# Optimization experiments

Hardware: AMD Instinct MI355X
Metric: run time of the kernel (lower is better)

Reference implementation:

```python
import jax, jax.numpy as jnp
import numpy as np

K_NN = 20  # neighbors per group (k=20 in source)


def fps_one(xyz, npoint):
    # xyz: [N,3] -> indices [npoint] via iterative furthest point sampling
    N = xyz.shape[0]
    def body(carry, _):
        dist, far = carry
        d = jnp.sum((xyz - xyz[far]) ** 2, axis=-1)
        dist = jnp.minimum(dist, d)
        return (dist, jnp.argmax(dist).astype(jnp.int32)), far
    init = (jnp.full((N,), 1e10, xyz.dtype), jnp.int32(0))
    _, idx = jax.lax.scan(body, init, None, length=npoint)
    return idx


def gather(pts, idx):
    # pts: [B,M,C], idx: [B,...] -> [B,...,C]
    return jax.vmap(lambda p, i: p[i])(pts, idx)


def knn(q, ref, k):
    # q: [B,S,3], ref: [B,M,3] -> [B,S,k] indices of nearest refs
    d = (jnp.sum(q * q, -1, keepdims=True)
         - 2.0 * jnp.einsum('bsc,bmc->bsm', q, ref)
         + jnp.sum(ref * ref, -1)[:, None, :])
    _, idx = jax.lax.top_k(-d, k)
    return idx


def sa_block(xyz, feats, npoint, W, b):
    # Set abstraction: FPS sample -> kNN group -> shared MLP -> max pool
    fidx = jax.vmap(fps_one, in_axes=(0, None))(xyz, npoint)   # [B,S]
    new_xyz = gather(xyz, fidx)                                 # [B,S,3]
    nidx = knn(new_xyz, xyz, K_NN)                              # [B,S,K]
    rel = gather(xyz, nidx) - new_xyz[:, :, None, :]            # [B,S,K,3]
    grp = jnp.concatenate([rel, gather(feats, nidx)], -1)       # [B,S,K,3+C]
    h = jax.nn.relu(jnp.einsum('bskc,cd->bskd', grp, W) + b)
    return new_xyz, jnp.max(h, axis=2)                          # [B,S,Cout]


def fp_block(xq, xr, fr, skip, W, b):
    # Feature propagation: 3-NN inverse-distance interp -> concat skip -> MLP
    idx = knn(xq, xr, 3)                                        # [B,S,3]
    d = jnp.sum((gather(xr, idx) - xq[:, :, None, :]) ** 2, -1)
    w = 1.0 / (d + 1e-8)
    w = w / jnp.sum(w, -1, keepdims=True)
    interp = jnp.einsum('bsk,bskc->bsc', w, gather(fr, idx))
    cat = jnp.concatenate([interp, skip], -1)
    return jax.nn.relu(jnp.einsum('bsc,cd->bsd', cat, W) + b)


def setup_inputs() -> dict:
    key = jax.random.key(0)
    ks = jax.random.split(key, 24)
    B, N = 8, 4096
    x = jax.random.normal(ks[0], (B, 6, N), jnp.float32)
    cls_label = jax.random.uniform(ks[1], (B, 16), jnp.float32)
    def lin(k, cin, cout):
        kw, kb = jax.random.split(k)
        s = 1.0 / np.sqrt(cin)
        return (jax.random.normal(kw, (cin, cout), jnp.float32) * s,
                jax.random.normal(kb, (cout,), jnp.float32) * 0.01)
    W0, b0 = lin(ks[2], 6, 64)
    W1, b1 = lin(ks[3], 67, 128)
    W2, b2 = lin(ks[4], 131, 256)
    W3, b3 = lin(ks[5], 259, 512)
    F3, fb3 = lin(ks[6], 768, 512)
    F2, fb2 = lin(ks[7], 640, 256)
    F1, fb1 = lin(ks[8], 320, 128)
    F0, fb0 = lin(ks[9], 150, 128)
    Wseg, bseg = lin(ks[10], 128, 50)
    return {"x": x, "cls_label": cls_label,
            "W0": W0, "b0": b0, "W1": W1, "b1": b1, "W2": W2, "b2": b2,
            "W3": W3, "b3": b3, "F3": F3, "fb3": fb3, "F2": F2, "fb2": fb2,
            "F1": F1, "fb1": fb1, "F0": F0, "fb0": fb0,
            "Wseg": Wseg, "bseg": bseg}


def reference(x, cls_label, W0, b0, W1, b1, W2, b2, W3, b3,
              F3, fb3, F2, fb2, F1, fb1, F0, fb0, Wseg, bseg):
    B, _, N = x.shape
    xyz = jnp.transpose(x[:, :3, :], (0, 2, 1))   # [B,N,3]
    nrm = jnp.transpose(x[:, 3:, :], (0, 2, 1))   # [B,N,3]
    # hierarchical set abstraction (512 -> 256 -> 128 -> 64 points)
    x1, f1 = sa_block(xyz, nrm, 512, W0, b0)      # f1: [B,512,64]
    x2, f2 = sa_block(x1, f1, 256, W1, b1)        # f2: [B,256,128]
    x3, f3 = sa_block(x2, f2, 128, W2, b2)        # f3: [B,128,256]
    x4, f4 = sa_block(x3, f3, 64, W3, b3)         # f4: [B,64,512]
    # feature propagation back up
    g3 = fp_block(x3, x4, f4, f3, F3, fb3)        # [B,128,512]
    g2 = fp_block(x2, x3, g3, f2, F2, fb2)        # [B,256,256]
    g1 = fp_block(x1, x2, g2, f1, F1, fb1)        # [B,512,128]
    cls = jnp.broadcast_to(cls_label[:, None, :], (B, N, 16))
    skip0 = jnp.concatenate([cls, xyz, nrm], -1)  # [B,N,22]
    g0 = fp_block(xyz, x1, g1, skip0, F0, fb0)    # [B,N,128]
    result = jnp.einsum('bnc,cd->bnd', g0, Wseg) + bseg  # [B,N,50]
    return result, jnp.transpose(g0, (0, 2, 1))
```

## Files before the change

kernel.cpp:

```cpp
#include <hip/hip_runtime.h>
#include <float.h>

#define B8 8
#define NPTS 4096

__global__ void split_xyz_kernel(const float* __restrict__ x,
                                 float* __restrict__ xyz, float* __restrict__ nrm) {
  int g = blockIdx.x * 256 + threadIdx.x;
  if (g >= B8 * NPTS) return;
  int b = g / NPTS, n = g % NPTS;
  const float* xb = x + (size_t)b * 6 * NPTS;
  float* o1 = xyz + (size_t)g * 3;
  float* o2 = nrm + (size_t)g * 3;
  o1[0] = xb[0 * NPTS + n]; o1[1] = xb[1 * NPTS + n]; o1[2] = xb[2 * NPTS + n];
  o2[0] = xb[3 * NPTS + n]; o2[1] = xb[4 * NPTS + n]; o2[2] = xb[5 * NPTS + n];
}

template <int CTRL, int RM>
__device__ __forceinline__ unsigned dppmov(unsigned v) {
  return (unsigned)__builtin_amdgcn_update_dpp((int)v, (int)v, CTRL, RM, 0xf, false);
}

template <int CTRL, int RM>
__device__ __forceinline__ void red_key_max(unsigned& kh, unsigned& kl) {
  unsigned oh = dppmov<CTRL, RM>(kh);
  unsigned ol = dppmov<CTRL, RM>(kl);
  unsigned long long ko = ((unsigned long long)oh << 32) | ol;
  unsigned long long k  = ((unsigned long long)kh << 32) | kl;
  bool c = ko > k;
  kh = c ? oh : kh;
  kl = c ? ol : kl;
}

template <int CTRL, int RM>
__device__ __forceinline__ void red_key_min(unsigned& kh, unsigned& kl) {
  unsigned oh = dppmov<CTRL, RM>(kh);
  unsigned ol = dppmov<CTRL, RM>(kl);
  unsigned long long ko = ((unsigned long long)oh << 32) | ol;
  unsigned long long k  = ((unsigned long long)kh << 32) | kl;
  bool c = ko < k;
  kh = c ? oh : kh;
  kl = c ? ol : kl;
}

#define WAVE_RED_MAX(kh, kl)            \
  red_key_max<0x111, 0xf>(kh, kl);      \
  red_key_max<0x112, 0xf>(kh, kl);      \
  red_key_max<0x114, 0xf>(kh, kl);      \
  red_key_max<0x118, 0xf>(kh, kl);      \
  red_key_max<0x142, 0xa>(kh, kl);      \
  red_key_max<0x143, 0xc>(kh, kl);

#define WAVE_RED_MIN(kh, kl)            \
  red_key_min<0x111, 0xf>(kh, kl);      \
  red_key_min<0x112, 0xf>(kh, kl);      \
  red_key_min<0x114, 0xf>(kh, kl);      \
  red_key_min<0x118, 0xf>(kh, kl);      \
  red_key_min<0x142, 0xa>(kh, kl);      \
  red_key_min<0x143, 0xc>(kh, kl);

template <int BLOCK, int P>
__global__ __launch_bounds__(BLOCK) void fps4_kernel(const float* __restrict__ xyz,
                                                     int N, int S,
                                                     float* __restrict__ out_xyz) {
#pragma clang fp contract(off)
  constexpr int NW = BLOCK / 64;
  __shared__ float4 pts[BLOCK * P];
  __shared__ float4 sel[512];
  __shared__ alignas(16) unsigned long long wkey[2][NW];
  int b = blockIdx.x, t = threadIdx.x;
  const float* p = xyz + (size_t)b * N * 3;
  float px[P], py[P], pz[P], dist[P];
#pragma unroll
  for (int j = 0; j < P; ++j) {
    int idx = t + j * BLOCK;
    float a = p[3 * idx], bb = p[3 * idx + 1], c = p[3 * idx + 2];
    px[j] = a; py[j] = bb; pz[j] = c;
    pts[idx] = make_float4(a, bb, c, 0.f);
    dist[j] = 1e10f;
  }
  __syncthreads();
  float fx = p[0], fy = p[1], fz = p[2];
  for (int i = 0; i < S; ++i) {
    if (t == 0) sel[i] = make_float4(fx, fy, fz, 0.f);
    float bv = -1.0f;
    int bj = 0;
#pragma unroll
    for (int j = 0; j < P; ++j) {
      float dx = px[j] - fx, dy = py[j] - fy, dz = pz[j] - fz;
      float d = dx * dx + dy * dy + dz * dz;
      float nd = fminf(dist[j], d);
      dist[j] = nd;
      bool c = nd > bv;
      bv = c ? nd : bv;
      bj = c ? j : bj;
    }
    unsigned kh = __float_as_uint(bv);
    unsigned kl = (unsigned)(~(t + bj * BLOCK));
    WAVE_RED_MAX(kh, kl);
    int buf = i & 1;
    if ((t & 63) == 63)
      wkey[buf][t >> 6] = ((unsigned long long)kh << 32) | kl;
    __syncthreads();
    unsigned long long g = 0ull;
    const ulonglong2* wk2 = (const ulonglong2*)&wkey[buf][0];
#pragma unroll
    for (int w = 0; w < NW / 2; ++w) {
      ulonglong2 e = wk2[w];
      unsigned long long m = (e.x > e.y) ? e.x : e.y;
      g = (m > g) ? m : g;
    }
    int far = (int)~(unsigned)g;
    float4 f = pts[far];
    fx = f.x; fy = f.y; fz = f.z;
  }
  __syncthreads();
  for (int i = t; i < S; i += BLOCK) {
    float4 f = sel[i];
    float* o = out_xyz + ((size_t)b * S + i) * 3;
    o[0] = f.x; o[1] = f.y; o[2] = f.z;
  }
}

__global__ __launch_bounds__(64) void knn20_kernel(const float* __restrict__ q,
                                                   const float* __restrict__ ref,
                                                   int S, int M, int* __restrict__ nidx,
                                                   int LDQ, int LDR) {
#pragma clang fp contract(off)
  int bs = blockIdx.x;
  int b = bs / S, s = bs % S;
  int t = threadIdx.x;
  __shared__ float sd[4096];
  const float* qp = q + ((size_t)b * LDQ + s) * 3;
  float qx = qp[0], qy = qp[1], qz = qp[2];
  float qq = qx * qx + qy * qy + qz * qz;
  const float* rp = ref + (size_t)b * LDR * 3;
  for (int i = t; i < M; i += 64) {
    float rx = rp[3 * i], ry = rp[3 * i + 1], rz = rp[3 * i + 2];
    float rr = rx * rx + ry * ry + rz * rz;
    float dot = qx * rx + qy * ry + qz * rz;
    sd[i] = qq - 2.0f * dot + rr;
  }
  __syncthreads();
  unsigned keep = 0;
  for (int k = 0; k < 20; ++k) {
    float bv = FLT_MAX;
    int bi = 0;
    for (int i = t; i < M; i += 64) {
      float v = sd[i];
      bool c = v < bv;
      bv = c ? v : bv;
      bi = c ? i : bi;
    }
    unsigned kh = __float_as_uint(bv), kl = (unsigned)bi;
    WAVE_RED_MIN(kh, kl);
    unsigned w = (unsigned)__builtin_amdgcn_readlane((int)kl, 63);
    if (t == k) keep = w;
    if (t == 0) sd[w] = FLT_MAX;
    __syncthreads();
  }
  if (t < 20) nidx[(size_t)bs * 20 + t] = (int)keep;
}

__device__ __forceinline__ void knn3_store(int g, const float* rx3,
                                           float qx, float qy, float qz,
                                           int i0, int i1, int i2,
                                           int* __restrict__ idx3,
                                           float* __restrict__ w3) {
#pragma clang fp contract(off)
  int ii[3] = {i0, i1, i2};
  float w[3];
  float wsum = 0.0f;
#pragma unroll
  for (int k = 0; k < 3; ++k) {
    const float* r = rx3 + (size_t)ii[k] * 3;
    float dx = r[0] - qx, dy = r[1] - qy, dz = r[2] - qz;
    float d = dx * dx + dy * dy + dz * dz;
    w[k] = 1.0f / (d + 1e-8f);
    wsum += w[k];
  }
#pragma unroll
  for (int k = 0; k < 3; ++k) {
    idx3[(size_t)g * 3 + k] = ii[k];
    w3[(size_t)g * 3 + k] = w[k] / wsum;
  }
}

__global__ __launch_bounds__(256) void neighbors_kernel(
    const float* __restrict__ xyz, const float* __restrict__ x1,
    int* __restrict__ nidx2, int* __restrict__ nidx3, int* __restrict__ nidx4,
    int* __restrict__ idx3_3, float* __restrict__ w3_3,
    int* __restrict__ idx3_2, float* __restrict__ w3_2,
    int* __restrict__ idx3_1, float* __restrict__ w3_1,
    int* __restrict__ idx3_0, float* __restrict__ w3_0) {
#pragma clang fp contract(off)
  __shared__ float4 smem4[512];
  int blk = blockIdx.x, tid = threadIdx.x;

  if (blk < 896) {
    int S, M, qid;
    int* nout;
    const int wv = tid >> 6, t64 = tid & 63;
    if (blk < 512)      { S = 256; M = 512; qid = blk * 4 + wv;         nout = nidx2; }
    else if (blk < 768) { S = 128; M = 256; qid = (blk - 512) * 4 + wv; nout = nidx3; }
    else                { S = 64;  M = 128; qid = (blk - 768) * 4 + wv; nout = nidx4; }
    float* swd = (float*)smem4 + wv * M;
    int b = qid / S, s = qid % S;
    const float* qp = x1 + ((size_t)b * 512 + s) * 3;
    float qx = qp[0], qy = qp[1], qz = qp[2];
    float qq = qx * qx + qy * qy + qz * qz;
    const float* rp = x1 + (size_t)b * 512 * 3;
    for (int i = t64; i < M; i += 64) {
      float rx = rp[3 * i], ry = rp[3 * i + 1], rz = rp[3 * i + 2];
      float rr = rx * rx + ry * ry + rz * rz;
      float dot = qx * rx + qy * ry + qz * rz;
      swd[i] = qq - 2.0f * dot + rr;
    }
    __syncthreads();
    unsigned keep = 0;
    for (int k = 0; k < 20; ++k) {
      float bv = FLT_MAX;
      int bi = 0;
      for (int i = t64; i < M; i += 64) {
        float v = swd[i];
        bool c = v < bv;
        bv = c ? v : bv;
        bi = c ? i : bi;
      }
      unsigned kh = __float_as_uint(bv), kl = (unsigned)bi;
      WAVE_RED_MIN(kh, kl);
      unsigned w = (unsigned)__builtin_amdgcn_readlane((int)kl, 63);
      if (t64 == k) keep = w;
      if (t64 == 0) swd[w] = FLT_MAX;
      __syncthreads();
    }
    if (t64 < 20) nout[(size_t)qid * 20 + t64] = (int)keep;
    return;
  }

  if (blk < 900) {
    int g = (blk - 896) * 256 + tid;
    int Sq = 128, M = 64;
    int b = g / Sq, s = g % Sq;
    const float* qp = x1 + ((size_t)b * 512 + s) * 3;
    float qx = qp[0], qy = qp[1], qz = qp[2];
    float qq = qx * qx + qy * qy + qz * qz;
    const float* rp = x1 + (size_t)b * 512 * 3;
    float v0 = FLT_MAX, v1 = FLT_MAX, v2 = FLT_MAX;
    int i0 = 0, i1 = 0, i2 = 0;
    for (int i = 0; i < M; ++i) {
      float rx = rp[3 * i], ry = rp[3 * i + 1], rz = rp[3 * i + 2];
      float d = qq - 2.0f * (qx * rx + qy * ry + qz * rz) + (rx * rx + ry * ry + rz * rz);
      if (d < v2) {
        if (d < v1) {
          if (d < v0) { v2 = v1; i2 = i1; v1 = v0; i1 = i0; v0 = d; i0 = i; }
          else { v2 = v1; i2 = i1; v1 = d; i1 = i; }
        } else { v2 = d; i2 = i; }
      }
    }
    knn3_store(g, rp, qx, qy, qz, i0, i1, i2, idx3_3, w3_3);
    return;
  }

  int g, Sq, M, LDQ;
  int* oidx;
  float* ow;
  const float* q;
  if (blk < 908)      { g = (blk - 900) * 256 + tid; Sq = 256;  M = 128; oidx = idx3_2; ow = w3_2; q = x1;  LDQ = 512; }
  else if (blk < 924) { g = (blk - 908) * 256 + tid; Sq = 512;  M = 256; oidx = idx3_1; ow = w3_1; q = x1;  LDQ = 512; }
  else                { g = (blk - 924) * 256 + tid; Sq = 4096; M = 512; oidx = idx3_0; ow = w3_0; q = xyz; LDQ = 4096; }
  int b = g / Sq, s = g % Sq;
  const float* rp = x1 + (size_t)b * 512 * 3;
  for (int i = tid; i < M; i += 256) {
    float rx = rp[3 * i], ry = rp[3 * i + 1], rz = rp[3 * i + 2];
    smem4[i] = make_float4(rx, ry, rz, rx * rx + ry * ry + rz * rz);
  }
  __syncthreads();
  const float* qp = q + ((size_t)b * LDQ + s) * 3;
  float qx = qp[0], qy = qp[1], qz = qp[2];
  float qq = qx * qx + qy * qy + qz * qz;
  float v0 = FLT_MAX, v1 = FLT_MAX, v2 = FLT_MAX;
  int i0 = 0, i1 = 0, i2 = 0;
  for (int i = 0; i < M; ++i) {
    float4 r = smem4[i];
    float d = qq - 2.0f * (qx * r.x + qy * r.y + qz * r.z) + r.w;
    if (d < v2) {
      if (d < v1) {
        if (d < v0) { v2 = v1; i2 = i1; v1 = v0; i1 = i0; v0 = d; i0 = i; }
        else { v2 = v1; i2 = i1; v1 = d; i1 = i; }
      } else { v2 = d; i2 = i; }
    }
  }
  {
    int ii[3] = {i0, i1, i2};
    float w[3];
    float wsum = 0.0f;
#pragma unroll
    for (int k = 0; k < 3; ++k) {
      float4 r = smem4[ii[k]];
      float dx = r.x - qx, dy = r.y - qy, dz = r.z - qz;
      float d = dx * dx + dy * dy + dz * dz;
      w[k] = 1.0f / (d + 1e-8f);
      wsum += w[k];
    }
#pragma unroll
    for (int k = 0; k < 3; ++k) {
      oidx[(size_t)g * 3 + k] = ii[k];
      ow[(size_t)g * 3 + k] = w[k] / wsum;
    }
  }
}

#define GEMM_STAGE(k0v, ...)                                                      \
    {                                                                             \
      int r_ = (int)threadIdx.x & 63;                                             \
      int ks_ = (int)threadIdx.x >> 6;                                            \
      int rr = rowBase + r_;                                                      \
      int kq0 = (k0v) + ks_ * 4;                                                  \
      float4 va = make_float4(0.f, 0.f, 0.f, 0.f);                                \
      if (rr < Mrows) { __VA_ARGS__ }                                             \
      areg4 = va;                                                                 \
    }                                                                             \
    {                                                                             \
      int kk = (int)threadIdx.x >> 4;                                             \
      int n4 = ((int)threadIdx.x & 15) * 4;                                       \
      int kq = (k0v) + kk, cc = colBase + n4;                                     \
      if (colBase + 64 <= N) {                                                    \
        if (kq < K) breg4 = *reinterpret_cast<const float4*>(&Wm[(size_t)kq * N + cc]); \
        else breg4 = make_float4(0.f, 0.f, 0.f, 0.f);                             \
      } else {                                                                    \
        breg4.x = (kq < K && cc < N) ? Wm[(size_t)kq * N + cc] : 0.0f;            \
        breg4.y = (kq < K && cc + 1 < N) ? Wm[(size_t)kq * N + cc + 1] : 0.0f;    \
        breg4.z = (kq < K && cc + 2 < N) ? Wm[(size_t)kq * N + cc + 2] : 0.0f;    \
        breg4.w = (kq < K && cc + 3 < N) ? Wm[(size_t)kq * N + cc + 3] : 0.0f;    \
      }                                                                           \
    }

#define GEMM_WRITE_LDS(bufv)                                                      \
    {                                                                             \
      int r_ = (int)threadIdx.x & 63;                                             \
      int k4_ = ((int)threadIdx.x >> 6) * 4;                                      \
      As[bufv][k4_ + 0][r_] = areg4.x;                                            \
      As[bufv][k4_ + 1][r_] = areg4.y;                                            \
      As[bufv][k4_ + 2][r_] = areg4.z;                                            \
      As[bufv][k4_ + 3][r_] = areg4.w;                                            \
    }                                                                             \
    *reinterpret_cast<float4*>(&Bs[bufv][threadIdx.x >> 4][(threadIdx.x & 15) * 4]) = breg4;

#define GEMM_MAIN(...)                                                            \
  __shared__ alignas(16) float As[2][16][68];                                     \
  __shared__ alignas(16) float Bs[2][16][64];                                     \
  int tx = threadIdx.x & 15, ty = threadIdx.x >> 4;                               \
  int rowBase = blockIdx.y * 64;                                                  \
  int colBase = blockIdx.x * 64;                                                  \
  float acc[4][4] = {};                                                           \
  float4 areg4, breg4;                                                            \
  GEMM_STAGE(kLo, __VA_ARGS__)                                                    \
  GEMM_WRITE_LDS(0)                                                               \
  __syncthreads();                                                                \
  int cur = 0;                                                                    \
  for (int k0 = kLo; k0 < kHi; k0 += 16) {                                        \
    int nxt = cur ^ 1;                                                            \
    bool more = (k0 + 16 < kHi);                                                  \
    if (more) { GEMM_STAGE(k0 + 16, __VA_ARGS__) }                                \
    _Pragma("unroll")                                                             \
    for (int kk = 0; kk < 16; ++kk) {                                             \
      const float4 av = *reinterpret_cast<const float4*>(&As[cur][kk][ty * 4]);   \
      const float4 bv = *reinterpret_cast<const float4*>(&Bs[cur][kk][tx * 4]);   \
      acc[0][0] += av.x * bv.x; acc[0][1] += av.x * bv.y;                         \
      acc[0][2] += av.x * bv.z; acc[0][3] += av.x * bv.w;                         \
      acc[1][0] += av.y * bv.x; acc[1][1] += av.y * bv.y;                         \
      acc[1][2] += av.y * bv.z; acc[1][3] += av.y * bv.w;                         \
      acc[2][0] += av.z * bv.x; acc[2][1] += av.z * bv.y;                         \
      acc[2][2] += av.z * bv.z; acc[2][3] += av.z * bv.w;                         \
      acc[3][0] += av.w * bv.x; acc[3][1] += av.w * bv.y;                         \
      acc[3][2] += av.w * bv.z; acc[3][3] += av.w * bv.w;                         \
    }                                                                             \
    if (more) { GEMM_WRITE_LDS(nxt) }                                             \
    __syncthreads();                                                              \
    cur = nxt;                                                                    \
  }

#define GEMM_EPI_STORE                                                            \
  _Pragma("unroll")                                                               \
  for (int i = 0; i < 4; ++i) {                                                   \
    int row = rowBase + ty * 4 + i;                                               \
    if (row >= Mrows) continue;                                                   \
    _Pragma("unroll")                                                             \
    for (int j = 0; j < 4; ++j) {                                                 \
      int col = colBase + tx * 4 + j;                                             \
      if (col >= N) continue;                                                     \
      float v = acc[i][j] + bias[col];                                            \
      if (RELU) v = fmaxf(v, 0.0f);                                               \
      C[(size_t)row * N + col] = v;                                               \
    }                                                                             \
  }

__global__ __launch_bounds__(256) void gemm_kernel(const float* __restrict__ A,
                                                   const float* __restrict__ Wm,
                                                   const float* __restrict__ bias,
                                                   float* __restrict__ C,
                                                   int Mrows, int N, int K, int RELU) {
  const int kLo = 0, kHi = K;
  GEMM_MAIN(
    if (kq0 + 3 < K) {
      va = *reinterpret_cast<const float4*>(&A[(size_t)rr * K + kq0]);
    } else {
      va.x = (kq0 < K) ? A[(size_t)rr * K + kq0] : 0.0f;
      va.y = (kq0 + 1 < K) ? A[(size_t)rr * K + kq0 + 1] : 0.0f;
      va.z = (kq0 + 2 < K) ? A[(size_t)rr * K + kq0 + 2] : 0.0f;
      va.w = (kq0 + 3 < K) ? A[(size_t)rr * K + kq0 + 3] : 0.0f;
    }
  )
  GEMM_EPI_STORE
}

__global__ __launch_bounds__(256) void gemm_sa_kernel(
    const float* __restrict__ xyz, const float* __restrict__ feats,
    const float* __restrict__ new_xyz, const int* __restrict__ nidx,
    const float* __restrict__ Wm, const float* __restrict__ bias,
    float* __restrict__ fOut, int Mref, int LDR, int S, int LDQ, int Cf,
    int Mrows, int N, int K) {
  const int kLo = 0, kHi = K;
  GEMM_MAIN(
    int bs = rr / 20;
    int s_ = bs % S;
    int b = bs / S;
    int id = nidx[rr];
    const float* xr_ = xyz + ((size_t)b * LDR + id) * 3;
    const float* xq_ = new_xyz + ((size_t)b * LDQ + s_) * 3;
    const float* fb_ = feats + ((size_t)b * Mref + id) * Cf;
    float* vp_ = (float*)&va;
    _Pragma("unroll")
    for (int c_ = 0; c_ < 4; ++c_) {
      int kq = kq0 + c_;
      float v = 0.0f;
      if (kq < K) v = (kq < 3) ? (xr_[kq] - xq_[kq]) : fb_[kq - 3];
      vp_[c_] = v;
    }
  )
  __shared__ int smax[4][64];
  int gBase = rowBase / 20;
  int nG = (rowBase + 63) / 20 - gBase + 1;
  for (int l = threadIdx.x; l < nG * 64; l += 256) smax[l >> 6][l & 63] = 0;
  __syncthreads();
  {
    int gl = (rowBase + ty * 4) / 20 - gBase;
#pragma unroll
    for (int j = 0; j < 4; ++j) {
      int col = colBase + tx * 4 + j;
      if (col >= N) continue;
      float bb = bias[col];
      float m = 0.0f;
#pragma unroll
      for (int i = 0; i < 4; ++i) {
        int row = rowBase + ty * 4 + i;
        if (row >= Mrows) continue;
        m = fmaxf(m, fmaxf(acc[i][j] + bb, 0.0f));
      }
      atomicMax(&smax[gl][tx * 4 + j], __float_as_int(m));
    }
  }
  __syncthreads();
  for (int l = threadIdx.x; l < nG * 64; l += 256) {
    int g = gBase + (l >> 6), c = colBase + (l & 63);
    if (c < N) atomicMax((int*)&fOut[(size_t)g * N + c], smax[l >> 6][l & 63]);
  }
}

__global__ __launch_bounds__(256) void gemm_fp_kernel(
    const float* __restrict__ fr, const int* __restrict__ idx3,
    const float* __restrict__ w3, const float* __restrict__ skip,
    const float* __restrict__ cls, const float* __restrict__ xyzq,
    const float* __restrict__ nrmq, const float* __restrict__ frBias,
    const float* __restrict__ Wm, const float* __restrict__ bias,
    float* __restrict__ C, int Sq, int Mr, int Cr, int Cs, int mode,
    int SPLITK, int CHUNK,
    int Mrows, int N, int K) {
  const int kLo = blockIdx.z * CHUNK;
  const int kHi = min(K, kLo + CHUNK);
  GEMM_MAIN(
    int bs = rr;
    int b = bs / Sq;
    const int* ii_ = idx3 + (size_t)bs * 3;
    const float* ww_ = w3 + (size_t)bs * 3;
    int i0_ = ii_[0], i1_ = ii_[1], i2_ = ii_[2];
    float w0_ = ww_[0], w1_ = ww_[1], w2_ = ww_[2];
    const float* fb_ = fr + (size_t)b * Mr * Cr;
    float* vp_ = (float*)&va;
    _Pragma("unroll")
    for (int c_ = 0; c_ < 4; ++c_) {
      int kq = kq0 + c_;
      float v = 0.0f;
      if (kq < K) {
        if (kq < Cr) {
          float a0 = fb_[(size_t)i0_ * Cr + kq];
          float a1 = fb_[(size_t)i1_ * Cr + kq];
          float a2 = fb_[(size_t)i2_ * Cr + kq];
          if (frBias) {
            float bb = frBias[kq];
            a0 = fmaxf(a0 + bb, 0.0f);
            a1 = fmaxf(a1 + bb, 0.0f);
            a2 = fmaxf(a2 + bb, 0.0f);
          }
          v = w0_ * a0;
          v += w1_ * a1;
          v += w2_ * a2;
        } else {
          int cc = kq - Cr;
          if (mode == 0) {
            v = skip[(size_t)bs * Cs + cc];
          } else {
            if (cc < 16) v = cls[(size_t)b * 16 + cc];
            else if (cc < 19) v = xyzq[(size_t)bs * 3 + (cc - 16)];
            else v = nrmq[(size_t)bs * 3 + (cc - 19)];
          }
        }
      }
      vp_[c_] = v;
    }
  )
  if (SPLITK) {
#pragma unroll
    for (int i = 0; i < 4; ++i) {
      int row = rowBase + ty * 4 + i;
      if (row >= Mrows) continue;
#pragma unroll
      for (int j = 0; j < 4; ++j) {
        int col = colBase + tx * 4 + j;
        if (col >= N) continue;
        atomicAdd(&C[(size_t)row * N + col], acc[i][j]);
      }
    }
  } else {
    const int RELU = 1;
    GEMM_EPI_STORE
  }
}

__global__ __launch_bounds__(256) void transpose_g0_kernel(const float* __restrict__ g0,
                                                           float* __restrict__ out2) {
  __shared__ float tile[32][33];
  int n0 = blockIdx.x * 32, c0 = blockIdx.y * 32, b = blockIdx.z;
  int tx = threadIdx.x & 31, ty = threadIdx.x >> 5;
#pragma unroll
  for (int j = 0; j < 32; j += 8)
    tile[ty + j][tx] = g0[((size_t)b * NPTS + n0 + ty + j) * 128 + c0 + tx];
  __syncthreads();
#pragma unroll
  for (int j = 0; j < 32; j += 8)
    out2[((size_t)b * 128 + c0 + ty + j) * NPTS + n0 + tx] = tile[tx][ty + j];
}

static inline int cdiv(int a, int b) { return (a + b - 1) / b; }

extern "C" void kernel_launch(void* const* d_in, const int* in_sizes, int n_in,
                              void* d_out, int out_size, void* d_ws, size_t ws_size,
                              hipStream_t stream) {
  const float* x    = (const float*)d_in[0];
  const float* cls  = (const float*)d_in[1];
  const float* W0 = (const float*)d_in[2];  const float* b0 = (const float*)d_in[3];
  const float* W1 = (const float*)d_in[4];  const float* b1 = (const float*)d_in[5];
  const float* W2 = (const float*)d_in[6];  const float* b2 = (const float*)d_in[7];
  const float* W3 = (const float*)d_in[8];  const float* b3 = (const float*)d_in[9];
  const float* F3 = (const float*)d_in[10]; const float* fb3 = (const float*)d_in[11];
  const float* F2 = (const float*)d_in[12]; const float* fb2 = (const float*)d_in[13];
  const float* F1 = (const float*)d_in[14]; const float* fb1 = (const float*)d_in[15];
  const float* F0 = (const float*)d_in[16]; const float* fb0 = (const float*)d_in[17];
  const float* Wseg = (const float*)d_in[18]; const float* bseg = (const float*)d_in[19];
  float* out = (float*)d_out;

  float* ws = (float*)d_ws;
  size_t off = 0;
  auto alloc = [&](size_t n) { float* p = ws + off; off += (n + 3) & ~(size_t)3; return p; };
  float* xyz = alloc(8 * 4096 * 3);
  float* nrm = alloc(8 * 4096 * 3);
  float* x1 = alloc(8 * 512 * 3);
  float* f1 = alloc(8 * 512 * 64);
  float* f2 = alloc(8 * 256 * 128);
  float* f3 = alloc(8 * 128 * 256);
  float* f4 = alloc(8 * 64 * 512);
  float* g3 = alloc(8 * 128 * 512);
  float* g2 = alloc(8 * 256 * 256);
  float* g1 = alloc(8 * 512 * 128);
  float* g0 = alloc(8 * 4096 * 128);
  int* nidx1 = (int*)alloc(8 * 512 * 20);
  int* nidx2 = (int*)alloc(8 * 256 * 20);
  int* nidx3 = (int*)alloc(8 * 128 * 20);
  int* nidx4 = (int*)alloc(8 * 64 * 20);
  int* idx3_3 = (int*)alloc(8 * 128 * 3);  float* w3_3 = alloc(8 * 128 * 3);
  int* idx3_2 = (int*)alloc(8 * 256 * 3);  float* w3_2 = alloc(8 * 256 * 3);
  int* idx3_1 = (int*)alloc(8 * 512 * 3);  float* w3_1 = alloc(8 * 512 * 3);
  int* idx3_0 = (int*)alloc(8 * 4096 * 3); float* w3_0 = alloc(8 * 4096 * 3);

  hipMemsetAsync(f1, 0,
                 ((size_t)8 * (512 * 64 + 256 * 128 + 128 * 256 + 64 * 512) +
                  (size_t)8 * (128 * 512 + 256 * 256 + 512 * 128)) * 4, stream);

  split_xyz_kernel<<<cdiv(8 * 4096, 256), 256, 0, stream>>>(x, xyz, nrm);
  fps4_kernel<256, 16><<<8, 256, 0, stream>>>(xyz, 4096, 512, x1);
  knn20_kernel<<<8 * 512, 64, 0, stream>>>(x1, xyz, 512, 4096, nidx1, 512, 4096);
  neighbors_kernel<<<1052, 256, 0, stream>>>(xyz, x1, nidx2, nidx3, nidx4,
                                             idx3_3, w3_3, idx3_2, w3_2,
                                             idx3_1, w3_1, idx3_0, w3_0);

  {
    dim3 grid(1, cdiv(8 * 512 * 20, 64));
    gemm_sa_kernel<<<grid, 256, 0, stream>>>(xyz, nrm, x1, nidx1, W0, b0, f1,
                                             4096, 4096, 512, 512, 3,
                                             8 * 512 * 20, 64, 6);
  }
  {
    dim3 grid(2, cdiv(8 * 256 * 20, 64));
    gemm_sa_kernel<<<grid, 256, 0, stream>>>(x1, f1, x1, nidx2, W1, b1, f2,
                                             512, 512, 256, 512, 64,
                                             8 * 256 * 20, 128, 67);
  }
  {
    dim3 grid(4, cdiv(8 * 128 * 20, 64));
    gemm_sa_kernel<<<grid, 256, 0, stream>>>(x1, f2, x1, nidx3, W2, b2, f3,
                                             256, 512, 128, 512, 128,
                                             8 * 128 * 20, 256, 131);
  }
  {
    dim3 grid(8, cdiv(8 * 64 * 20, 64));
    gemm_sa_kernel<<<grid, 256, 0, stream>>>(x1, f3, x1, nidx4, W3, b3, f4,
                                             128, 512, 64, 512, 256,
                                             8 * 64 * 20, 512, 259);
  }

  {
    dim3 grid(8, cdiv(8 * 128, 64), 4);
    gemm_fp_kernel<<<grid, 256, 0, stream>>>(f4, idx3_3, w3_3, f3, nullptr, nullptr, nullptr,
                                             nullptr, F3, fb3, g3, 128, 64, 512, 256, 0,
                                             1, 192, 8 * 128, 512, 768);
  }
  {
    dim3 grid(4, cdiv(8 * 256, 64), 4);
    gemm_fp_kernel<<<grid, 256, 0, stream>>>(g3, idx3_2, w3_2, f2, nullptr, nullptr, nullptr,
                                             fb3, F2, fb2, g2, 256, 128, 512, 128, 0,
                                             1, 160, 8 * 256, 256, 640);
  }
  {
    dim3 grid(2, cdiv(8 * 512, 64), 2);
    gemm_fp_kernel<<<grid, 256, 0, stream>>>(g2, idx3_1, w3_1, f1, nullptr, nullptr, nullptr,
                                             fb2, F1, fb1, g1, 512, 256, 256, 64, 0,
                                             1, 160, 8 * 512, 128, 320);
  }
  {
    dim3 grid(2, cdiv(8 * 4096, 64), 1);
    gemm_fp_kernel<<<grid, 256, 0, stream>>>(g1, idx3_0, w3_0, nullptr, cls, xyz, nrm,
                                             fb1, F0, fb0, g0, 4096, 512, 128, 22, 1,
                                             0, 160, 8 * 4096, 128, 150);
  }

  {
    dim3 grid(1, cdiv(8 * 4096, 64));
    gemm_kernel<<<grid, 256, 0, stream>>>(g0, Wseg, bseg, out, 8 * 4096, 50, 128, 0);
  }
  transpose_g0_kernel<<<dim3(128, 4, 8), 256, 0, stream>>>(g0, out + (size_t)8 * 4096 * 50);
}
```

Measured before the change: 1.039 ms.

## Speed up kNN-20 with per-lane top-2 caching and dedicated SA1 kernel

Precomputes a float4 xyz array with the squared norm so the kNN-20 kernel does one vector load per reference point. Each lane keeps its two best candidates while distances are written, so the 20 selection rounds only rescan the lane that lost its winner instead of rescanning all 4096 distances every round. The first set-abstraction MLP moves from the generic gather-GEMM kernel to a specialized kernel, one wave per group, that computes the 6-input dot products and max-pools them directly. The trade-off is extra memory for the float4 buffer, plus possible divergence when one lane must rescan its slice.

```diff
diff --git a/kernel.cpp b/kernel.cpp
--- a/kernel.cpp
+++ b/kernel.cpp
@@ -5,14 +5,18 @@
 #define NPTS 4096
 
 __global__ void split_xyz_kernel(const float* __restrict__ x,
-                                 float* __restrict__ xyz, float* __restrict__ nrm) {
+                                 float* __restrict__ xyz, float* __restrict__ nrm,
+                                 float4* __restrict__ xyz4) {
+#pragma clang fp contract(off)
   int g = blockIdx.x * 256 + threadIdx.x;
   if (g >= B8 * NPTS) return;
   int b = g / NPTS, n = g % NPTS;
   const float* xb = x + (size_t)b * 6 * NPTS;
   float* o1 = xyz + (size_t)g * 3;
   float* o2 = nrm + (size_t)g * 3;
-  o1[0] = xb[0 * NPTS + n]; o1[1] = xb[1 * NPTS + n]; o1[2] = xb[2 * NPTS + n];
+  float a0 = xb[0 * NPTS + n], a1 = xb[1 * NPTS + n], a2 = xb[2 * NPTS + n];
+  o1[0] = a0; o1[1] = a1; o1[2] = a2;
+  xyz4[g] = make_float4(a0, a1, a2, a0 * a0 + a1 * a1 + a2 * a2);
   o2[0] = xb[3 * NPTS + n]; o2[1] = xb[4 * NPTS + n]; o2[2] = xb[5 * NPTS + n];
 }
 
@@ -123,43 +127,95 @@
 }
 
 __global__ __launch_bounds__(64) void knn20_kernel(const float* __restrict__ q,
-                                                   const float* __restrict__ ref,
-                                                   int S, int M, int* __restrict__ nidx,
-                                                   int LDQ, int LDR) {
+                                                   const float4* __restrict__ ref4,
+                                                   int* __restrict__ nidx) {
 #pragma clang fp contract(off)
   int bs = blockIdx.x;
-  int b = bs / S, s = bs % S;
+  int b = bs >> 9;
   int t = threadIdx.x;
   __shared__ float sd[4096];
-  const float* qp = q + ((size_t)b * LDQ + s) * 3;
+  const float* qp = q + (size_t)bs * 3;
   float qx = qp[0], qy = qp[1], qz = qp[2];
   float qq = qx * qx + qy * qy + qz * qz;
-  const float* rp = ref + (size_t)b * LDR * 3;
-  for (int i = t; i < M; i += 64) {
-    float rx = rp[3 * i], ry = rp[3 * i + 1], rz = rp[3 * i + 2];
-    float rr = rx * rx + ry * ry + rz * rz;
-    float dot = qx * rx + qy * ry + qz * rz;
-    sd[i] = qq - 2.0f * dot + rr;
+  const float4* rp = ref4 + (size_t)b * 4096;
+  float v1 = FLT_MAX, v2 = FLT_MAX;
+  int i1 = 0, i2 = 0;
+  for (int k = 0; k < 64; ++k) {
+    int i = t + (k << 6);
+    float4 r = rp[i];
+    float dot = qx * r.x + qy * r.y + qz * r.z;
+    float d = qq - 2.0f * dot + r.w;
+    sd[i] = d;
+    if (d < v1) { v2 = v1; i2 = i1; v1 = d; i1 = i; }
+    else if (d < v2) { v2 = d; i2 = i; }
   }
   __syncthreads();
   unsigned keep = 0;
   for (int k = 0; k < 20; ++k) {
-    float bv = FLT_MAX;
-    int bi = 0;
-    for (int i = t; i < M; i += 64) {
-      float v = sd[i];
-      bool c = v < bv;
-      bv = c ? v : bv;
-      bi = c ? i : bi;
-    }
-    unsigned kh = __float_as_uint(bv), kl = (unsigned)bi;
+    unsigned kh = __float_as_uint(v1), kl = (unsigned)i1;
     WAVE_RED_MIN(kh, kl);
     unsigned w = (unsigned)__builtin_amdgcn_readlane((int)kl, 63);
     if (t == k) keep = w;
     if (t == 0) sd[w] = FLT_MAX;
     __syncthreads();
+    if (((int)w & 63) == t) {
+      v1 = v2; i1 = i2;
+      v2 = FLT_MAX; i2 = 0;
+      if (v1 == FLT_MAX) {
+        for (int kk = 0; kk < 64; ++kk) {
+          int i = t + (kk << 6);
+          float d = sd[i];
+          if (d < v1) { v2 = v1; i2 = i1; v1 = d; i1 = i; }
+          else if (d < v2) { v2 = d; i2 = i; }
+        }
+      }
+    }
   }
   if (t < 20) nidx[(size_t)bs * 20 + t] = (int)keep;
+}
+
+__global__ __launch_bounds__(256) void sa1_kernel(
+    const float* __restrict__ xyz, const float* __restrict__ nrm,
+    const float* __restrict__ x1, const int* __restrict__ nidx,
+    const float* __restrict__ W, const float* __restrict__ bias,
+    float* __restrict__ f1) {
+#pragma clang fp contract(off)
+  __shared__ alignas(16) float smem_in[4][20][8];
+  int wv = threadIdx.x >> 6, t = threadIdx.x & 63;
+  int g = blockIdx.x * 4 + wv;
+  int b = g >> 9;
+  if (t < 20) {
+    int id = nidx[(size_t)g * 20 + t];
+    const float* xr = xyz + ((size_t)b * 4096 + id) * 3;
+    const float* xq = x1 + (size_t)g * 3;
+    const float* nr = nrm + ((size_t)b * 4096 + id) * 3;
+    smem_in[wv][t][0] = xr[0] - xq[0];
+    smem_in[wv][t][1] = xr[1] - xq[1];
+    smem_in[wv][t][2] = xr[2] - xq[2];
+    smem_in[wv][t][3] = nr[0];
+    smem_in[wv][t][4] = nr[1];
+    smem_in[wv][t][5] = nr[2];
+    smem_in[wv][t][6] = 0.0f;
+    smem_in[wv][t][7] = 0.0f;
+  }
+  __syncthreads();
+  float w0 = W[0 * 64 + t], w1 = W[1 * 64 + t], w2 = W[2 * 64 + t];
+  float w3 = W[3 * 64 + t], w4 = W[4 * 64 + t], w5 = W[5 * 64 + t];
+  float bb = bias[t];
+  float m = 0.0f;
+  for (int n = 0; n < 20; ++n) {
+    const float4 a = *reinterpret_cast<const float4*>(&smem_in[wv][n][0]);
+    const float4 c = *reinterpret_cast<const float4*>(&smem_in[wv][n][4]);
+    float v = a.x * w0;
+    v += a.y * w1;
+    v += a.z * w2;
+    v += a.w * w3;
+    v += c.x * w4;
+    v += c.y * w5;
+    v += bb;
+    m = fmaxf(m, v);
+  }
+  f1[(size_t)g * 64 + t] = m;
 }
 
 __device__ __forceinline__ void knn3_store(int g, const float* rx3,
@@ -575,6 +631,7 @@
   auto alloc = [&](size_t n) { float* p = ws + off; off += (n + 3) & ~(size_t)3; return p; };
   float* xyz = alloc(8 * 4096 * 3);
   float* nrm = alloc(8 * 4096 * 3);
+  float4* xyz4 = (float4*)alloc(8 * 4096 * 4);
   float* x1 = alloc(8 * 512 * 3);
   float* f1 = alloc(8 * 512 * 64);
   float* f2 = alloc(8 * 256 * 128);
@@ -597,19 +654,14 @@
                  ((size_t)8 * (512 * 64 + 256 * 128 + 128 * 256 + 64 * 512) +
                   (size_t)8 * (128 * 512 + 256 * 256 + 512 * 128)) * 4, stream);
 
-  split_xyz_kernel<<<cdiv(8 * 4096, 256), 256, 0, stream>>>(x, xyz, nrm);
+  split_xyz_kernel<<<cdiv(8 * 4096, 256), 256, 0, stream>>>(x, xyz, nrm, xyz4);
   fps4_kernel<256, 16><<<8, 256, 0, stream>>>(xyz, 4096, 512, x1);
-  knn20_kernel<<<8 * 512, 64, 0, stream>>>(x1, xyz, 512, 4096, nidx1, 512, 4096);
+  knn20_kernel<<<8 * 512, 64, 0, stream>>>(x1, xyz4, nidx1);
+  sa1_kernel<<<1024, 256, 0, stream>>>(xyz, nrm, x1, nidx1, W0, b0, f1);
   neighbors_kernel<<<1052, 256, 0, stream>>>(xyz, x1, nidx2, nidx3, nidx4,
                                              idx3_3, w3_3, idx3_2, w3_2,
                                              idx3_1, w3_1, idx3_0, w3_0);
 
-  {
-    dim3 grid(1, cdiv(8 * 512 * 20, 64));
-    gemm_sa_kernel<<<grid, 256, 0, stream>>>(xyz, nrm, x1, nidx1, W0, b0, f1,
-                                             4096, 4096, 512, 512, 3,
-                                             8 * 512 * 20, 64, 6);
-  }
   {
     dim3 grid(2, cdiv(8 * 256 * 20, 64));
     gemm_sa_kernel<<<grid, 256, 0, stream>>>(x1, f1, x1, nidx2, W1, b1, f2,
```

Measured after the change: 960.9 us. 7.6% less time.
